# Performance work log

Measured on AMD Instinct MI355X. Metric: run time of the kernel, lower is better.

## Reference

```python
import math
import jax, jax.numpy as jnp
import numpy as np

B, S, D, H = 4, 2048, 1024, 16
DK = D // H
THETA = 10000.0


def _rope(xh, pos):
    # xh: [B, H, S, DK], pos: [S]
    half = jnp.arange(0, DK, 2, dtype=jnp.float32) / DK
    inv_freq = THETA ** (-half)                      # [DK/2]
    ang = pos.astype(jnp.float32)[:, None] * inv_freq  # [S, DK/2]
    cos, sin = jnp.cos(ang).astype(xh.dtype), jnp.sin(ang).astype(xh.dtype)
    x1, x2 = xh[..., 0::2], xh[..., 1::2]
    r1 = x1 * cos - x2 * sin
    r2 = x1 * sin + x2 * cos
    return jnp.stack([r1, r2], axis=-1).reshape(xh.shape)


def setup_inputs() -> dict:
    key = jax.random.key(0)
    kx, kq, kk, kv, ko = jax.random.split(key, 5)
    std = 0.02
    x = jax.random.normal(kx, (B, S, D), jnp.float32)
    wq = jax.random.normal(kq, (D, D), jnp.float32) * std
    wk = jax.random.normal(kk, (D, D), jnp.float32) * std
    wv = jax.random.normal(kv, (D, D), jnp.float32) * std
    wo = jax.random.normal(ko, (D, D), jnp.float32) * std
    token_positions = jnp.arange(S, dtype=jnp.int32)
    return {"x": x, "wq": wq, "wk": wk, "wv": wv, "wo": wo,
            "token_positions": token_positions}


def reference(x, wq, wk, wv, wo, token_positions):
    # bias-free linear projections: y = x @ W^T (torch Linear convention)
    q = x @ wq.T
    k = x @ wk.T
    v = x @ wv.T
    # split heads: [B, S, D] -> [B, H, S, DK]
    to_heads = lambda t: t.reshape(B, S, H, DK).transpose(0, 2, 1, 3)
    qh, kh, vh = to_heads(q), to_heads(k), to_heads(v)
    qh = _rope(qh, token_positions)
    kh = _rope(kh, token_positions)
    scores = jnp.einsum('bhqd,bhkd->bhqk', qh, kh) / math.sqrt(DK)
    causal = jnp.tril(jnp.ones((S, S), dtype=bool))
    scores = jnp.where(causal, scores, -jnp.inf)
    attn = jax.nn.softmax(scores, axis=-1)
    out = jnp.einsum('bhqk,bhkd->bhqd', attn, vh)       # [B, H, S, DK]
    out = out.transpose(0, 2, 1, 3).reshape(B, S, D)    # merge heads
    return out @ wo.T
```

## Files before the change

kernel.cpp:

```cpp
#include <hip/hip_runtime.h>

#define B_ 4
#define S_ 2048
#define D_ 1024
#define H_ 16
#define DK_ 64
#define M_ (B_*S_)
#define K_ D_
#define N_ D_

typedef unsigned short u16;
typedef unsigned int u32;
typedef __bf16 bf16x8 __attribute__((ext_vector_type(8)));
typedef float f32x4 __attribute__((ext_vector_type(4)));
typedef u32 u32x4v __attribute__((ext_vector_type(4)));

#define EXP2F(x) __builtin_amdgcn_exp2f(x)

__device__ __forceinline__ u16 f2bf(float f) {
    u32 u = __builtin_bit_cast(u32, f);
    u += 0x7fff + ((u >> 16) & 1);
    return (u16)(u >> 16);
}
__device__ __forceinline__ float bf2f(u16 h) {
    u32 u = ((u32)h) << 16;
    return __builtin_bit_cast(float, u);
}
__device__ __forceinline__ u32 pack_trunc(float a, float b) {
    return (__builtin_bit_cast(u32, a) >> 16) | (__builtin_bit_cast(u32, b) & 0xffff0000u);
}

#define GLDS16(g, l) __builtin_amdgcn_global_load_lds( \
    (__attribute__((address_space(1))) void*)(g),      \
    (__attribute__((address_space(3))) void*)(l), 16, 0, 0)

__global__ __launch_bounds__(256) void cvt_x(const float* __restrict__ in,
                                             u16* __restrict__ out, int n4) {
    const int i = blockIdx.x * 256 + threadIdx.x;
    if (i >= n4) return;
    const float4 f = *(const float4*)(in + (size_t)i * 4);
    u32 p0 = (u32)f2bf(f.x) | ((u32)f2bf(f.y) << 16);
    u32 p1 = (u32)f2bf(f.z) | ((u32)f2bf(f.w) << 16);
    *(uint2*)(out + (size_t)i * 4) = make_uint2(p0, p1);
}

__global__ __launch_bounds__(256) void cvt_w4(
    const float* __restrict__ w0, const float* __restrict__ w1,
    const float* __restrict__ w2, const float* __restrict__ w3,
    u16* __restrict__ o0, u16* __restrict__ o1,
    u16* __restrict__ o2, u16* __restrict__ o3) {
    const int wi = blockIdx.y;
    const float* in = (wi == 0) ? w0 : (wi == 1) ? w1 : (wi == 2) ? w2 : w3;
    u16* out       = (wi == 0) ? o0 : (wi == 1) ? o1 : (wi == 2) ? o2 : o3;
    const int i = blockIdx.x * 256 + threadIdx.x;
    const float4 f = *(const float4*)(in + (size_t)i * 4);
    u32 p0 = (u32)f2bf(f.x) | ((u32)f2bf(f.y) << 16);
    u32 p1 = (u32)f2bf(f.z) | ((u32)f2bf(f.w) << 16);
    *(uint2*)(out + (size_t)i * 4) = make_uint2(p0, p1);
}

template <int MODE>
__device__ __forceinline__ void gemm_tile(const u16* __restrict__ A,
                                          const u16* __restrict__ Bm,
                                          void* __restrict__ Cv,
                                          int m0, int n0) {
    __shared__ u16 As[2][128 * 32];
    __shared__ u16 Bs[2][128 * 32];
    const int tid  = threadIdx.x;
    const int wave = tid >> 6, lane = tid & 63;
    const int wm = wave & 1, wn = wave >> 1;
    const int quad = lane >> 4, mcol = lane & 15;

    const int c0 = wave, c1 = wave + 4;
    const int r0 = c0 * 16 + (lane >> 2), r1 = c1 * 16 + (lane >> 2);
    const int kb = (((lane & 3) ^ ((lane >> 3) & 3)) * 8);
    const u16* ga0 = A  + (size_t)(m0 + r0) * K_ + kb;
    const u16* ga1 = A  + (size_t)(m0 + r1) * K_ + kb;
    const u16* gb0 = Bm + (size_t)(n0 + r0) * K_ + kb;
    const u16* gb1 = Bm + (size_t)(n0 + r1) * K_ + kb;
    const int lo0 = c0 * 512, lo1 = c1 * 512;
    const int rsw = ((mcol >> 1) & 3);

    f32x4 acc[4][4];
#pragma unroll
    for (int i = 0; i < 4; i++)
#pragma unroll
        for (int j = 0; j < 4; j++) acc[i][j] = f32x4{0.f, 0.f, 0.f, 0.f};

    GLDS16(ga0, &As[0][lo0]); GLDS16(ga1, &As[0][lo1]);
    GLDS16(gb0, &Bs[0][lo0]); GLDS16(gb1, &Bs[0][lo1]);
    ga0 += 32; ga1 += 32; gb0 += 32; gb1 += 32;
    __syncthreads();

    for (int kt = 0; kt < K_; kt += 32) {
        const int cur = (kt >> 5) & 1;
        if (kt + 32 < K_) {
            const int nxt = cur ^ 1;
            GLDS16(ga0, &As[nxt][lo0]); GLDS16(ga1, &As[nxt][lo1]);
            GLDS16(gb0, &Bs[nxt][lo0]); GLDS16(gb1, &Bs[nxt][lo1]);
            ga0 += 32; ga1 += 32; gb0 += 32; gb1 += 32;
        }

        bf16x8 af[4], bfr[4];
#pragma unroll
        for (int i = 0; i < 4; i++) {
            af[i]  = *(const bf16x8*)&As[cur][(wm * 64 + i * 16 + mcol) * 32 + ((quad ^ rsw)) * 8];
            bfr[i] = *(const bf16x8*)&Bs[cur][(wn * 64 + i * 16 + mcol) * 32 + ((quad ^ rsw)) * 8];
        }
#pragma unroll
        for (int i = 0; i < 4; i++)
#pragma unroll
            for (int j = 0; j < 4; j++)
                acc[i][j] = __builtin_amdgcn_mfma_f32_16x16x32_bf16(
                    af[i], bfr[j], acc[i][j], 0, 0, 0);

        __syncthreads();
    }

#pragma unroll
    for (int i = 0; i < 4; i++) {
        const int row = m0 + wm * 64 + i * 16 + quad * 4;
#pragma unroll
        for (int j = 0; j < 4; j++) {
            const int col = n0 + wn * 64 + j * 16 + mcol;
            if constexpr (MODE == 2) {
                const int hh = col >> 6, dd = col & 63;
                const int bb = row >> 11, ss = row & 2047;
                const u32 lo = (u32)f2bf(acc[i][j][0]) | ((u32)f2bf(acc[i][j][1]) << 16);
                const u32 hi = (u32)f2bf(acc[i][j][2]) | ((u32)f2bf(acc[i][j][3]) << 16);
                *(uint2*)((u16*)Cv + ((size_t)((bb * H_ + hh) * DK_ + dd)) * S_ + ss) =
                    make_uint2(lo, hi);
            } else {
#pragma unroll
                for (int r = 0; r < 4; r++) {
                    if constexpr (MODE == 1)
                        ((float*)Cv)[(size_t)(row + r) * N_ + col] = acc[i][j][r];
                    else
                        ((u16*)Cv)[(size_t)(row + r) * N_ + col] = f2bf(acc[i][j][r]);
                }
            }
        }
    }
}

__global__ __launch_bounds__(256) void gemm_qkv_kernel(
    const u16* __restrict__ x,
    const u16* __restrict__ wq, const u16* __restrict__ wk,
    const u16* __restrict__ wv,
    u16* __restrict__ q, u16* __restrict__ k, u16* __restrict__ vt) {
    const int flat = blockIdx.x;
    const int w = (flat & 7) * 192 + (flat >> 3);
    const int my = w / 24;
    const int rem = w - my * 24;
    const int z = rem >> 3, nx = rem & 7;
    const int m0 = my * 128, n0 = nx * 128;
    if (z == 2) {
        gemm_tile<2>(x, wv, vt, m0, n0);
    } else {
        const u16* Bm = z ? wk : wq;
        u16* C        = z ? k  : q;
        gemm_tile<0>(x, Bm, C, m0, n0);
    }
}

__global__ __launch_bounds__(256) void gemm_out_kernel(
    const u16* __restrict__ o, const u16* __restrict__ wo, float* __restrict__ out) {
    const int flat = blockIdx.x;
    const int w = (flat & 7) * 64 + (flat >> 3);
    const int my = w >> 3, nx = w & 7;
    gemm_tile<1>(o, wo, out, my * 128, nx * 128);
}

__global__ __launch_bounds__(256) void rope_qk(u16* __restrict__ q,
                                               u16* __restrict__ k,
                                               const int* __restrict__ pos) {
    const int idx = blockIdx.x * 256 + threadIdx.x;
    const int seg = idx & 3;
    const int h = (idx >> 2) & (H_ - 1);
    const int s = (idx >> 6) & (S_ - 1);
    const int b = idx >> 17;
    const float p = (float)pos[s];
    const float QSC = 0.18033688011112042f;
    const size_t off = ((size_t)(b * S_ + s)) * D_ + h * DK_ + seg * 16;

    u32 qa[8], ka[8];
    *(uint4*)&qa[0] = *(const uint4*)(q + off);
    *(uint4*)&qa[4] = *(const uint4*)(q + off + 8);
    *(uint4*)&ka[0] = *(const uint4*)(k + off);
    *(uint4*)&ka[4] = *(const uint4*)(k + off + 8);
#pragma unroll
    for (int w = 0; w < 8; w++) {
        const int i = seg * 8 + w;
        const float inv = exp2f((float)i * (-13.287712379549449f / 32.f));
        const float ang = p * inv;
        float sn, cs;
        __sincosf(ang, &sn, &cs);
        {
            const float x1 = bf2f((u16)(qa[w] & 0xffff));
            const float x2 = bf2f((u16)(qa[w] >> 16));
            qa[w] = (u32)f2bf((x1 * cs - x2 * sn) * QSC) |
                    ((u32)f2bf((x1 * sn + x2 * cs) * QSC) << 16);
        }
        {
            const float x1 = bf2f((u16)(ka[w] & 0xffff));
            const float x2 = bf2f((u16)(ka[w] >> 16));
            ka[w] = (u32)f2bf(x1 * cs - x2 * sn) |
                    ((u32)f2bf(x1 * sn + x2 * cs) << 16);
        }
    }
    *(uint4*)(q + off)     = *(uint4*)&qa[0];
    *(uint4*)(q + off + 8) = *(uint4*)&qa[4];
    *(uint4*)(k + off)     = *(uint4*)&ka[0];
    *(uint4*)(k + off + 8) = *(uint4*)&ka[4];
}

__global__ __launch_bounds__(256) void attn_kernel(
    const u16* __restrict__ q, const u16* __restrict__ k,
    const u16* __restrict__ vt, u16* __restrict__ o) {
    __shared__ u16 Ks[64 * 64];
    __shared__ u16 Vs[64 * 64];

    const int tid = threadIdx.x, wave = tid >> 6, lane = tid & 63;
    const int flat = blockIdx.x;
    const int qp = flat >> 6;
    const int h = flat & (H_ - 1);
    const int b = (flat >> 4) & 3;
    const int quad = lane >> 4, mcol = lane & 15;
    const int srd = mcol & 7;

    const int rr2 = tid >> 2, cc2 = tid & 3;
    const int sw = rr2 & 7;
    const int so0 = rr2 * 64 + (((cc2 * 2)     ^ sw) << 3);
    const int so1 = rr2 * 64 + (((cc2 * 2 + 1) ^ sw) << 3);
    const int prr = (rr2 & 35) | ((rr2 & 12) << 1) | ((rr2 & 16) >> 2);
    const int ch2 = cc2 * 16;
    const u16* krow = k + ((size_t)(b * S_ + prr)) * D_ + h * DK_ + ch2;
    const u16* vrow = vt + ((size_t)((b * H_ + h) * DK_ + rr2)) * S_ + ch2;

    for (int pass = 0; pass < 2; pass++) {
        const int qt = pass ? (15 - qp) : qp;
        const int q0 = qt * 128;
        const int wq0 = q0 + wave * 32;
        const int jmax = 2 * qt + 1;

        bf16x8 qf[2][2];
#pragma unroll
        for (int g = 0; g < 2; g++) {
            const u16* qs = q + ((size_t)(b * S_ + wq0 + g * 16 + mcol)) * D_ + h * DK_ + quad * 8;
            qf[g][0] = *(const bf16x8*)qs;
            qf[g][1] = *(const bf16x8*)(qs + 32);
        }

        float m[2] = {-1e30f, -1e30f}, l[2] = {0.f, 0.f};
        f32x4 oacc[2][4];
#pragma unroll
        for (int g = 0; g < 2; g++)
#pragma unroll
            for (int dn = 0; dn < 4; dn++) oacc[g][dn] = f32x4{0.f, 0.f, 0.f, 0.f};

        uint4 kr0 = *(const uint4*)(krow);
        uint4 kr1 = *(const uint4*)(krow + 8);
        uint4 vr0 = *(const uint4*)(vrow);
        uint4 vr1 = *(const uint4*)(vrow + 8);

        for (int j = 0; j <= jmax; j++) {
            __syncthreads();
            *(uint4*)&Ks[so0] = kr0;
            *(uint4*)&Ks[so1] = kr1;
            *(uint4*)&Vs[so0] = vr0;
            *(uint4*)&Vs[so1] = vr1;
            __syncthreads();

            if (j < jmax) {
                kr0 = *(const uint4*)(krow + (size_t)(j + 1) * 64 * D_);
                kr1 = *(const uint4*)(krow + (size_t)(j + 1) * 64 * D_ + 8);
                vr0 = *(const uint4*)(vrow + (j + 1) * 64);
                vr1 = *(const uint4*)(vrow + (j + 1) * 64 + 8);
            }

            if (j * 64 > wq0 + 31) continue;

            f32x4 st[2][4];
            __builtin_amdgcn_s_setprio(1);
#pragma unroll
            for (int n = 0; n < 4; n++) {
                const u16* kl = &Ks[(n * 16 + mcol) * 64];
                bf16x8 kf0 = *(const bf16x8*)&kl[(quad ^ srd) << 3];
                bf16x8 kf1 = *(const bf16x8*)&kl[((quad | 4) ^ srd) << 3];
                f32x4 z0 = f32x4{0.f, 0.f, 0.f, 0.f};
                z0 = __builtin_amdgcn_mfma_f32_16x16x32_bf16(kf0, qf[0][0], z0, 0, 0, 0);
                z0 = __builtin_amdgcn_mfma_f32_16x16x32_bf16(kf1, qf[0][1], z0, 0, 0, 0);
                st[0][n] = z0;
                f32x4 z1 = f32x4{0.f, 0.f, 0.f, 0.f};
                z1 = __builtin_amdgcn_mfma_f32_16x16x32_bf16(kf0, qf[1][0], z1, 0, 0, 0);
                z1 = __builtin_amdgcn_mfma_f32_16x16x32_bf16(kf1, qf[1][1], z1, 0, 0, 0);
                st[1][n] = z1;
            }
            __builtin_amdgcn_s_setprio(0);

            if (j * 64 + 63 > wq0) {
#pragma unroll
                for (int g = 0; g < 2; g++) {
                    const int qg = wq0 + g * 16 + mcol;
#pragma unroll
                    for (int n = 0; n < 4; n++) {
                        const int tb = j * 64 + ((n >> 1) << 5) + ((n & 1) << 2) + quad * 8;
#pragma unroll
                        for (int r = 0; r < 4; r++)
                            if (tb + r > qg) st[g][n][r] = -1e30f;
                    }
                }
            }

#pragma unroll
            for (int g = 0; g < 2; g++) {
                float mx = st[g][0][0];
#pragma unroll
                for (int n = 0; n < 4; n++)
#pragma unroll
                    for (int r = 0; r < 4; r++) mx = fmaxf(mx, st[g][n][r]);
                mx = fmaxf(mx, __shfl_xor(mx, 16));
                mx = fmaxf(mx, __shfl_xor(mx, 32));
                float al = 1.f;
                const bool need = !__all(mx <= m[g] + 8.f);
                if (need) {
                    const float mnew = fmaxf(m[g], mx);
                    al = EXP2F(m[g] - mnew);
                    m[g] = mnew;
                }
                float sum = 0.f;
#pragma unroll
                for (int n = 0; n < 4; n++)
#pragma unroll
                    for (int r = 0; r < 4; r++) {
                        const float p = EXP2F(st[g][n][r] - m[g]);
                        st[g][n][r] = p;
                        sum += p;
                    }
                sum += __shfl_xor(sum, 16);
                sum += __shfl_xor(sum, 32);
                l[g] = l[g] * al + sum;
                if (need) {
                    float alphaT[4];
#pragma unroll
                    for (int r = 0; r < 4; r++) alphaT[r] = __shfl(al, quad * 4 + r);
#pragma unroll
                    for (int dn = 0; dn < 4; dn++)
#pragma unroll
                        for (int r = 0; r < 4; r++) oacc[g][dn][r] *= alphaT[r];
                }
            }

            bf16x8 pf[2][2];
#pragma unroll
            for (int g = 0; g < 2; g++) {
                u32x4v w0, w1;
                w0[0] = pack_trunc(st[g][0][0], st[g][0][1]);
                w0[1] = pack_trunc(st[g][0][2], st[g][0][3]);
                w0[2] = pack_trunc(st[g][1][0], st[g][1][1]);
                w0[3] = pack_trunc(st[g][1][2], st[g][1][3]);
                w1[0] = pack_trunc(st[g][2][0], st[g][2][1]);
                w1[1] = pack_trunc(st[g][2][2], st[g][2][3]);
                w1[2] = pack_trunc(st[g][3][0], st[g][3][1]);
                w1[3] = pack_trunc(st[g][3][2], st[g][3][3]);
                pf[g][0] = __builtin_bit_cast(bf16x8, w0);
                pf[g][1] = __builtin_bit_cast(bf16x8, w1);
            }

            __builtin_amdgcn_s_setprio(1);
#pragma unroll
            for (int dn = 0; dn < 4; dn++) {
                const u16* vl = &Vs[(dn * 16 + mcol) * 64];
                bf16x8 vf0 = *(const bf16x8*)&vl[(quad ^ srd) << 3];
                bf16x8 vf1 = *(const bf16x8*)&vl[((quad | 4) ^ srd) << 3];
#pragma unroll
                for (int g = 0; g < 2; g++) {
                    oacc[g][dn] = __builtin_amdgcn_mfma_f32_16x16x32_bf16(pf[g][0], vf0, oacc[g][dn], 0, 0, 0);
                    oacc[g][dn] = __builtin_amdgcn_mfma_f32_16x16x32_bf16(pf[g][1], vf1, oacc[g][dn], 0, 0, 0);
                }
            }
            __builtin_amdgcn_s_setprio(0);
        }

#pragma unroll
        for (int g = 0; g < 2; g++) {
            float linv[4];
#pragma unroll
            for (int r = 0; r < 4; r++) linv[r] = 1.f / __shfl(l[g], quad * 4 + r);
#pragma unroll
            for (int dn = 0; dn < 4; dn++)
#pragma unroll
                for (int r = 0; r < 4; r++) {
                    const int row = wq0 + g * 16 + quad * 4 + r;
                    o[((size_t)(b * S_ + row)) * D_ + h * DK_ + dn * 16 + mcol] =
                        f2bf(oacc[g][dn][r] * linv[r]);
                }
        }
    }
}

extern "C" void kernel_launch(void* const* d_in, const int* in_sizes, int n_in,
                              void* d_out, int out_size, void* d_ws, size_t ws_size,
                              hipStream_t stream) {
    const float* x  = (const float*)d_in[0];
    const float* wq = (const float*)d_in[1];
    const float* wk = (const float*)d_in[2];
    const float* wv = (const float*)d_in[3];
    const float* wo = (const float*)d_in[4];
    const int*   tp = (const int*)d_in[5];
    float* out = (float*)d_out;

    u16* ws = (u16*)d_ws;
    const size_t NE = (size_t)M_ * D_;
    const size_t WE = (size_t)N_ * K_;
    u16* xb  = ws;
    u16* wqb = ws + NE;
    u16* wkb = wqb + WE;
    u16* wvb = wkb + WE;
    u16* wob = wvb + WE;
    u16* qb  = wob + WE;
    u16* kb  = qb + NE;
    u16* vtb = (u16*)d_out;
    u16* ob  = xb;

    dim3 blk(256);
    cvt_x<<<dim3((int)(NE / 1024)), blk, 0, stream>>>(x, xb, (int)(NE / 4));
    cvt_w4<<<dim3((int)(WE / 1024), 4), blk, 0, stream>>>(wq, wk, wv, wo, wqb, wkb, wvb, wob);

    gemm_qkv_kernel<<<dim3(3 * (M_ / 128) * (N_ / 128)), blk, 0, stream>>>(xb, wqb, wkb, wvb, qb, kb, vtb);
    rope_qk<<<dim3((B_ * S_ * H_ * 4) / 256), blk, 0, stream>>>(qb, kb, tp);
    attn_kernel<<<dim3((S_ / 128 / 2) * H_ * B_), blk, 0, stream>>>(qb, kb, vtb, ob);
    gemm_out_kernel<<<dim3((M_ / 128) * (N_ / 128)), blk, 0, stream>>>(ob, wob, out);
}
```

Before: 266.9 us.

## Restructure attention into 64-row query tiles with 2-wave blocks and MFMA row sums

The attention kernel drops the paired-pass scheme, in which each 4-wave block handled two 128-row query tiles. Each 2-wave block now handles one 64-row query tile, with heavier tiles scheduled first, giving 4x more blocks and a finer load balance. The softmax row sum is now computed with an MFMA against a ones vector instead of cross-lane shuffles. Each thread also loads twice as much K/V into shared memory. In exchange, K/V reuse per block is lower: the same K/V tiles are loaded by more blocks.

```diff
diff --git a/kernel.cpp b/kernel.cpp
--- a/kernel.cpp
+++ b/kernel.cpp
@@ -214,7 +214,7 @@
     *(uint4*)(k + off + 8) = *(uint4*)&ka[4];
 }
 
-__global__ __launch_bounds__(256) void attn_kernel(
+__global__ __launch_bounds__(128, 4) void attn_kernel(
     const u16* __restrict__ q, const u16* __restrict__ k,
     const u16* __restrict__ vt, u16* __restrict__ o) {
     __shared__ u16 Ks[64 * 64];
@@ -222,180 +222,184 @@
 
     const int tid = threadIdx.x, wave = tid >> 6, lane = tid & 63;
     const int flat = blockIdx.x;
-    const int qp = flat >> 6;
+    const int qt = 31 - (flat >> 6);
     const int h = flat & (H_ - 1);
     const int b = (flat >> 4) & 3;
     const int quad = lane >> 4, mcol = lane & 15;
     const int srd = mcol & 7;
-
-    const int rr2 = tid >> 2, cc2 = tid & 3;
+    const int q0 = qt * 64;
+    const int wq0 = q0 + wave * 32;
+    const int jmax = qt;
+
+    const int rr2 = tid >> 1, cc2 = tid & 1;
     const int sw = rr2 & 7;
-    const int so0 = rr2 * 64 + (((cc2 * 2)     ^ sw) << 3);
-    const int so1 = rr2 * 64 + (((cc2 * 2 + 1) ^ sw) << 3);
+    int so[4];
+#pragma unroll
+    for (int t = 0; t < 4; t++)
+        so[t] = rr2 * 64 + (((cc2 * 4 + t) ^ sw) << 3);
     const int prr = (rr2 & 35) | ((rr2 & 12) << 1) | ((rr2 & 16) >> 2);
-    const int ch2 = cc2 * 16;
+    const int ch2 = cc2 * 32;
     const u16* krow = k + ((size_t)(b * S_ + prr)) * D_ + h * DK_ + ch2;
     const u16* vrow = vt + ((size_t)((b * H_ + h) * DK_ + rr2)) * S_ + ch2;
 
-    for (int pass = 0; pass < 2; pass++) {
-        const int qt = pass ? (15 - qp) : qp;
-        const int q0 = qt * 128;
-        const int wq0 = q0 + wave * 32;
-        const int jmax = 2 * qt + 1;
-
-        bf16x8 qf[2][2];
+    u32x4v onesw;
+    onesw[0] = onesw[1] = onesw[2] = onesw[3] = 0x3F803F80u;
+    const bf16x8 onesf = __builtin_bit_cast(bf16x8, onesw);
+
+    bf16x8 qf[2][2];
+#pragma unroll
+    for (int g = 0; g < 2; g++) {
+        const u16* qs = q + ((size_t)(b * S_ + wq0 + g * 16 + mcol)) * D_ + h * DK_ + quad * 8;
+        qf[g][0] = *(const bf16x8*)qs;
+        qf[g][1] = *(const bf16x8*)(qs + 32);
+    }
+
+    float m[2] = {-1e30f, -1e30f};
+    f32x4 lacc[2];
+    f32x4 oacc[2][4];
+#pragma unroll
+    for (int g = 0; g < 2; g++) {
+        lacc[g] = f32x4{0.f, 0.f, 0.f, 0.f};
+#pragma unroll
+        for (int dn = 0; dn < 4; dn++) oacc[g][dn] = f32x4{0.f, 0.f, 0.f, 0.f};
+    }
+
+    uint4 kr[4], vr[4];
+#pragma unroll
+    for (int t = 0; t < 4; t++) {
+        kr[t] = *(const uint4*)(krow + t * 8);
+        vr[t] = *(const uint4*)(vrow + t * 8);
+    }
+
+    for (int j = 0; j <= jmax; j++) {
+        __syncthreads();
+#pragma unroll
+        for (int t = 0; t < 4; t++) {
+            *(uint4*)&Ks[so[t]] = kr[t];
+            *(uint4*)&Vs[so[t]] = vr[t];
+        }
+        __syncthreads();
+
+        if (j < jmax) {
+#pragma unroll
+            for (int t = 0; t < 4; t++) {
+                kr[t] = *(const uint4*)(krow + (size_t)(j + 1) * 64 * D_ + t * 8);
+                vr[t] = *(const uint4*)(vrow + (j + 1) * 64 + t * 8);
+            }
+        }
+
+        f32x4 st[2][4];
+        __builtin_amdgcn_s_setprio(1);
+#pragma unroll
+        for (int n = 0; n < 4; n++) {
+            const u16* kl = &Ks[(n * 16 + mcol) * 64];
+            bf16x8 kf0 = *(const bf16x8*)&kl[(quad ^ srd) << 3];
+            bf16x8 kf1 = *(const bf16x8*)&kl[((quad | 4) ^ srd) << 3];
+            f32x4 z0 = f32x4{0.f, 0.f, 0.f, 0.f};
+            z0 = __builtin_amdgcn_mfma_f32_16x16x32_bf16(kf0, qf[0][0], z0, 0, 0, 0);
+            z0 = __builtin_amdgcn_mfma_f32_16x16x32_bf16(kf1, qf[0][1], z0, 0, 0, 0);
+            st[0][n] = z0;
+            f32x4 z1 = f32x4{0.f, 0.f, 0.f, 0.f};
+            z1 = __builtin_amdgcn_mfma_f32_16x16x32_bf16(kf0, qf[1][0], z1, 0, 0, 0);
+            z1 = __builtin_amdgcn_mfma_f32_16x16x32_bf16(kf1, qf[1][1], z1, 0, 0, 0);
+            st[1][n] = z1;
+        }
+        __builtin_amdgcn_s_setprio(0);
+
+        if (j == jmax) {
+#pragma unroll
+            for (int g = 0; g < 2; g++) {
+                const int qg = wq0 + g * 16 + mcol;
+#pragma unroll
+                for (int n = 0; n < 4; n++) {
+                    const int tb = j * 64 + ((n >> 1) << 5) + ((n & 1) << 2) + quad * 8;
+#pragma unroll
+                    for (int r = 0; r < 4; r++)
+                        if (tb + r > qg) st[g][n][r] = -1e30f;
+                }
+            }
+        }
+
 #pragma unroll
         for (int g = 0; g < 2; g++) {
-            const u16* qs = q + ((size_t)(b * S_ + wq0 + g * 16 + mcol)) * D_ + h * DK_ + quad * 8;
-            qf[g][0] = *(const bf16x8*)qs;
-            qf[g][1] = *(const bf16x8*)(qs + 32);
-        }
-
-        float m[2] = {-1e30f, -1e30f}, l[2] = {0.f, 0.f};
-        f32x4 oacc[2][4];
-#pragma unroll
-        for (int g = 0; g < 2; g++)
-#pragma unroll
-            for (int dn = 0; dn < 4; dn++) oacc[g][dn] = f32x4{0.f, 0.f, 0.f, 0.f};
-
-        uint4 kr0 = *(const uint4*)(krow);
-        uint4 kr1 = *(const uint4*)(krow + 8);
-        uint4 vr0 = *(const uint4*)(vrow);
-        uint4 vr1 = *(const uint4*)(vrow + 8);
-
-        for (int j = 0; j <= jmax; j++) {
-            __syncthreads();
-            *(uint4*)&Ks[so0] = kr0;
-            *(uint4*)&Ks[so1] = kr1;
-            *(uint4*)&Vs[so0] = vr0;
-            *(uint4*)&Vs[so1] = vr1;
-            __syncthreads();
-
-            if (j < jmax) {
-                kr0 = *(const uint4*)(krow + (size_t)(j + 1) * 64 * D_);
-                kr1 = *(const uint4*)(krow + (size_t)(j + 1) * 64 * D_ + 8);
-                vr0 = *(const uint4*)(vrow + (j + 1) * 64);
-                vr1 = *(const uint4*)(vrow + (j + 1) * 64 + 8);
-            }
-
-            if (j * 64 > wq0 + 31) continue;
-
-            f32x4 st[2][4];
-            __builtin_amdgcn_s_setprio(1);
-#pragma unroll
-            for (int n = 0; n < 4; n++) {
-                const u16* kl = &Ks[(n * 16 + mcol) * 64];
-                bf16x8 kf0 = *(const bf16x8*)&kl[(quad ^ srd) << 3];
-                bf16x8 kf1 = *(const bf16x8*)&kl[((quad | 4) ^ srd) << 3];
-                f32x4 z0 = f32x4{0.f, 0.f, 0.f, 0.f};
-                z0 = __builtin_amdgcn_mfma_f32_16x16x32_bf16(kf0, qf[0][0], z0, 0, 0, 0);
-                z0 = __builtin_amdgcn_mfma_f32_16x16x32_bf16(kf1, qf[0][1], z0, 0, 0, 0);
-                st[0][n] = z0;
-                f32x4 z1 = f32x4{0.f, 0.f, 0.f, 0.f};
-                z1 = __builtin_amdgcn_mfma_f32_16x16x32_bf16(kf0, qf[1][0], z1, 0, 0, 0);
-                z1 = __builtin_amdgcn_mfma_f32_16x16x32_bf16(kf1, qf[1][1], z1, 0, 0, 0);
-                st[1][n] = z1;
-            }
-            __builtin_amdgcn_s_setprio(0);
-
-            if (j * 64 + 63 > wq0) {
-#pragma unroll
-                for (int g = 0; g < 2; g++) {
-                    const int qg = wq0 + g * 16 + mcol;
-#pragma unroll
-                    for (int n = 0; n < 4; n++) {
-                        const int tb = j * 64 + ((n >> 1) << 5) + ((n & 1) << 2) + quad * 8;
-#pragma unroll
-                        for (int r = 0; r < 4; r++)
-                            if (tb + r > qg) st[g][n][r] = -1e30f;
-                    }
-                }
-            }
-
+            float mx = st[g][0][0];
+#pragma unroll
+            for (int n = 0; n < 4; n++)
+#pragma unroll
+                for (int r = 0; r < 4; r++) mx = fmaxf(mx, st[g][n][r]);
+            mx = fmaxf(mx, __shfl_xor(mx, 16));
+            mx = fmaxf(mx, __shfl_xor(mx, 32));
+            const bool need = !__all(mx <= m[g] + 8.f);
+            if (need) {
+                const float mnew = fmaxf(m[g], mx);
+                const float al = EXP2F(m[g] - mnew);
+                m[g] = mnew;
+                float alphaT[4];
+#pragma unroll
+                for (int r = 0; r < 4; r++) alphaT[r] = __shfl(al, quad * 4 + r);
+#pragma unroll
+                for (int dn = 0; dn < 4; dn++)
+#pragma unroll
+                    for (int r = 0; r < 4; r++) oacc[g][dn][r] *= alphaT[r];
+#pragma unroll
+                for (int r = 0; r < 4; r++) lacc[g][r] *= alphaT[r];
+            }
+#pragma unroll
+            for (int n = 0; n < 4; n++)
+#pragma unroll
+                for (int r = 0; r < 4; r++)
+                    st[g][n][r] = EXP2F(st[g][n][r] - m[g]);
+        }
+
+        bf16x8 pf[2][2];
+#pragma unroll
+        for (int g = 0; g < 2; g++) {
+            u32x4v w0, w1;
+            w0[0] = pack_trunc(st[g][0][0], st[g][0][1]);
+            w0[1] = pack_trunc(st[g][0][2], st[g][0][3]);
+            w0[2] = pack_trunc(st[g][1][0], st[g][1][1]);
+            w0[3] = pack_trunc(st[g][1][2], st[g][1][3]);
+            w1[0] = pack_trunc(st[g][2][0], st[g][2][1]);
+            w1[1] = pack_trunc(st[g][2][2], st[g][2][3]);
+            w1[2] = pack_trunc(st[g][3][0], st[g][3][1]);
+            w1[3] = pack_trunc(st[g][3][2], st[g][3][3]);
+            pf[g][0] = __builtin_bit_cast(bf16x8, w0);
+            pf[g][1] = __builtin_bit_cast(bf16x8, w1);
+        }
+
+        __builtin_amdgcn_s_setprio(1);
+#pragma unroll
+        for (int g = 0; g < 2; g++) {
+            lacc[g] = __builtin_amdgcn_mfma_f32_16x16x32_bf16(pf[g][0], onesf, lacc[g], 0, 0, 0);
+            lacc[g] = __builtin_amdgcn_mfma_f32_16x16x32_bf16(pf[g][1], onesf, lacc[g], 0, 0, 0);
+        }
+#pragma unroll
+        for (int dn = 0; dn < 4; dn++) {
+            const u16* vl = &Vs[(dn * 16 + mcol) * 64];
+            bf16x8 vf0 = *(const bf16x8*)&vl[(quad ^ srd) << 3];
+            bf16x8 vf1 = *(const bf16x8*)&vl[((quad | 4) ^ srd) << 3];
 #pragma unroll
             for (int g = 0; g < 2; g++) {
-                float mx = st[g][0][0];
-#pragma unroll
-                for (int n = 0; n < 4; n++)
-#pragma unroll
-                    for (int r = 0; r < 4; r++) mx = fmaxf(mx, st[g][n][r]);
-                mx = fmaxf(mx, __shfl_xor(mx, 16));
-                mx = fmaxf(mx, __shfl_xor(mx, 32));
-                float al = 1.f;
-                const bool need = !__all(mx <= m[g] + 8.f);
-                if (need) {
-                    const float mnew = fmaxf(m[g], mx);
-                    al = EXP2F(m[g] - mnew);
-                    m[g] = mnew;
-                }
-                float sum = 0.f;
-#pragma unroll
-                for (int n = 0; n < 4; n++)
-#pragma unroll
-                    for (int r = 0; r < 4; r++) {
-                        const float p = EXP2F(st[g][n][r] - m[g]);
-                        st[g][n][r] = p;
-                        sum += p;
-                    }
-                sum += __shfl_xor(sum, 16);
-                sum += __shfl_xor(sum, 32);
-                l[g] = l[g] * al + sum;
-                if (need) {
-                    float alphaT[4];
-#pragma unroll
-                    for (int r = 0; r < 4; r++) alphaT[r] = __shfl(al, quad * 4 + r);
-#pragma unroll
-                    for (int dn = 0; dn < 4; dn++)
-#pragma unroll
-                        for (int r = 0; r < 4; r++) oacc[g][dn][r] *= alphaT[r];
-                }
-            }
-
-            bf16x8 pf[2][2];
-#pragma unroll
-            for (int g = 0; g < 2; g++) {
-                u32x4v w0, w1;
-                w0[0] = pack_trunc(st[g][0][0], st[g][0][1]);
-                w0[1] = pack_trunc(st[g][0][2], st[g][0][3]);
-                w0[2] = pack_trunc(st[g][1][0], st[g][1][1]);
-                w0[3] = pack_trunc(st[g][1][2], st[g][1][3]);
-                w1[0] = pack_trunc(st[g][2][0], st[g][2][1]);
-                w1[1] = pack_trunc(st[g][2][2], st[g][2][3]);
-                w1[2] = pack_trunc(st[g][3][0], st[g][3][1]);
-                w1[3] = pack_trunc(st[g][3][2], st[g][3][3]);
-                pf[g][0] = __builtin_bit_cast(bf16x8, w0);
-                pf[g][1] = __builtin_bit_cast(bf16x8, w1);
-            }
-
-            __builtin_amdgcn_s_setprio(1);
-#pragma unroll
-            for (int dn = 0; dn < 4; dn++) {
-                const u16* vl = &Vs[(dn * 16 + mcol) * 64];
-                bf16x8 vf0 = *(const bf16x8*)&vl[(quad ^ srd) << 3];
-                bf16x8 vf1 = *(const bf16x8*)&vl[((quad | 4) ^ srd) << 3];
-#pragma unroll
-                for (int g = 0; g < 2; g++) {
-                    oacc[g][dn] = __builtin_amdgcn_mfma_f32_16x16x32_bf16(pf[g][0], vf0, oacc[g][dn], 0, 0, 0);
-                    oacc[g][dn] = __builtin_amdgcn_mfma_f32_16x16x32_bf16(pf[g][1], vf1, oacc[g][dn], 0, 0, 0);
-                }
-            }
-            __builtin_amdgcn_s_setprio(0);
-        }
-
-#pragma unroll
-        for (int g = 0; g < 2; g++) {
-            float linv[4];
-#pragma unroll
-            for (int r = 0; r < 4; r++) linv[r] = 1.f / __shfl(l[g], quad * 4 + r);
-#pragma unroll
-            for (int dn = 0; dn < 4; dn++)
-#pragma unroll
-                for (int r = 0; r < 4; r++) {
-                    const int row = wq0 + g * 16 + quad * 4 + r;
-                    o[((size_t)(b * S_ + row)) * D_ + h * DK_ + dn * 16 + mcol] =
-                        f2bf(oacc[g][dn][r] * linv[r]);
-                }
-        }
+                oacc[g][dn] = __builtin_amdgcn_mfma_f32_16x16x32_bf16(pf[g][0], vf0, oacc[g][dn], 0, 0, 0);
+                oacc[g][dn] = __builtin_amdgcn_mfma_f32_16x16x32_bf16(pf[g][1], vf1, oacc[g][dn], 0, 0, 0);
+            }
+        }
+        __builtin_amdgcn_s_setprio(0);
+    }
+
+#pragma unroll
+    for (int g = 0; g < 2; g++) {
+        float linv[4];
+#pragma unroll
+        for (int r = 0; r < 4; r++) linv[r] = 1.f / lacc[g][r];
+#pragma unroll
+        for (int dn = 0; dn < 4; dn++)
+#pragma unroll
+            for (int r = 0; r < 4; r++) {
+                const int row = wq0 + g * 16 + quad * 4 + r;
+                o[((size_t)(b * S_ + row)) * D_ + h * DK_ + dn * 16 + mcol] =
+                    f2bf(oacc[g][dn][r] * linv[r]);
+            }
     }
 }
 
@@ -429,6 +433,6 @@
 
     gemm_qkv_kernel<<<dim3(3 * (M_ / 128) * (N_ / 128)), blk, 0, stream>>>(xb, wqb, wkb, wvb, qb, kb, vtb);
     rope_qk<<<dim3((B_ * S_ * H_ * 4) / 256), blk, 0, stream>>>(qb, kb, tp);
-    attn_kernel<<<dim3((S_ / 128 / 2) * H_ * B_), blk, 0, stream>>>(qb, kb, vtb, ob);
+    attn_kernel<<<dim3((S_ / 64) * H_ * B_), dim3(128), 0, stream>>>(qb, kb, vtb, ob);
     gemm_out_kernel<<<dim3((M_ / 128) * (N_ / 128)), blk, 0, stream>>>(ob, wob, out);
 }
```

Result: slower. 372.8 us (+39.7%).
